# Optimization experiments

Measured on AMD Instinct MI355X. Metric: run time of the kernel, lower is better.

The kernel has to match this reference:

```python
import jax, jax.numpy as jnp
import numpy as np

B, S, D, H = 4, 2048, 1024, 16
HD = D // H


def setup_inputs() -> dict:
    key = jax.random.key(0)
    ks = jax.random.split(key, 6)
    scale = 1.0 / np.sqrt(D)
    return {
        'x': jax.random.normal(ks[0], (B, S, D), dtype=jnp.float32),
        'wq': jax.random.normal(ks[1], (D, D), dtype=jnp.float32) * scale,
        'wk': jax.random.normal(ks[2], (D, D), dtype=jnp.float32) * scale,
        'wv': jax.random.normal(ks[3], (D, D), dtype=jnp.float32) * scale,
        'wo': jax.random.normal(ks[4], (D, D), dtype=jnp.float32) * scale,
        'wo_b': jnp.zeros((D,), dtype=jnp.float32),
    }


def reference(x, wq, wk, wv, wo, wo_b):
    b, s, _ = x.shape
    # Linear projections (torch Linear: x @ W.T), reshape to [b, h, s, hd]
    def proj(w):
        return jnp.einsum('bsd,ed->bse', x, w).reshape(b, s, H, HD).transpose(0, 2, 1, 3)
    q, k, v = proj(wq), proj(wk), proj(wv)
    scores = jnp.einsum('bhqd,bhkd->bhqk', q, k)  # [b,h,s,s]
    causal = jnp.triu(jnp.ones((s, s), dtype=bool), k=1)
    scores = jnp.where(causal, -jnp.inf, scores)
    attn = jax.nn.softmax(scores / np.sqrt(HD), axis=-1)
    ctx = jnp.einsum('bhqk,bhkd->bhqd', attn, v)  # [b,h,s,hd]
    ctx = ctx.transpose(0, 2, 1, 3).reshape(b, s, D)
    return jnp.einsum('bsd,ed->bse', ctx, wo) + wo_b
```

## Files before the change

kernel.cpp:

```cpp
#include <hip/hip_runtime.h>

#define SB 4
#define SS 2048
#define SD 1024
#define SH 16
#define SHD 64
#define SM (SB * SS)

typedef __bf16 bf16x8 __attribute__((ext_vector_type(8)));
typedef float f32x4 __attribute__((ext_vector_type(4)));

static __device__ __forceinline__ unsigned short f2bf(float x) {
    unsigned int u = __builtin_bit_cast(unsigned int, x);
    u += 0x7fffu + ((u >> 16) & 1u);
    return (unsigned short)(u >> 16);
}

static __device__ __forceinline__ float fast_exp2(float x) {
#if __has_builtin(__builtin_amdgcn_exp2f)
    return __builtin_amdgcn_exp2f(x);
#else
    return exp2f(x);
#endif
}

static __device__ __forceinline__ unsigned int pkhi(float a, float b) {
    return __builtin_amdgcn_perm(__builtin_bit_cast(unsigned int, a),
                                 __builtin_bit_cast(unsigned int, b), 0x07060302u);
}

typedef __attribute__((address_space(1))) void GV;
typedef __attribute__((address_space(3))) void LV;

static __device__ __forceinline__ void async16(const void* g, void* l) {
    __builtin_amdgcn_global_load_lds((GV*)g, (LV*)l, 16, 0, 0);
}

#define QSCALE 0.18033688011112042f

__global__ __launch_bounds__(256) void cast_all(
    const float* __restrict__ x,  const float* __restrict__ wq,
    const float* __restrict__ wk, const float* __restrict__ wv,
    const float* __restrict__ wo,
    unsigned short* __restrict__ xb, unsigned short* __restrict__ wqkv,
    unsigned short* __restrict__ wo16) {
    int base = blockIdx.x * 512 + threadIdx.x;
#pragma unroll
    for (int it = 0; it < 2; ++it) {
        int i = base + it * 256;
        const float4* src;
        ushort4* dst;
        if (i < 2097152) {
            src = reinterpret_cast<const float4*>(x) + i;
            dst = reinterpret_cast<ushort4*>(xb) + i;
        } else {
            int j = i - 2097152;
            int which = j >> 18;
            int r = j & 262143;
            if (which == 0) {
                src = reinterpret_cast<const float4*>(wq) + r;
                dst = reinterpret_cast<ushort4*>(wqkv) + r;
            } else if (which == 1) {
                src = reinterpret_cast<const float4*>(wk) + r;
                dst = reinterpret_cast<ushort4*>(wqkv) + 262144 + r;
            } else if (which == 2) {
                src = reinterpret_cast<const float4*>(wv) + r;
                dst = reinterpret_cast<ushort4*>(wqkv) + 524288 + r;
            } else {
                src = reinterpret_cast<const float4*>(wo) + r;
                dst = reinterpret_cast<ushort4*>(wo16) + r;
            }
        }
        float4 v = *src;
        ushort4 o;
        o.x = f2bf(v.x); o.y = f2bf(v.y); o.z = f2bf(v.z); o.w = f2bf(v.w);
        *dst = o;
    }
}

#define NT16 (SD / 64)

__device__ __forceinline__ void gemm_mainloop(
    const unsigned short* __restrict__ A,
    const unsigned short* __restrict__ Bt,
    int tileM, int tileN, int tid,
    unsigned short* As0, unsigned short* As1, unsigned short* As2,
    unsigned short* Bs0, unsigned short* Bs1,
    f32x4 (&acc)[4][4]) {

    const int lane = tid & 63;
    const int quad = lane >> 4;
    const int col0 = lane & 15;
    const int w = tid >> 6;
    const int wm = w >> 1;
    const int wn = w & 1;

    const int r0 = tid >> 3;
    const int cc = ((tid & 7) ^ (r0 & 7)) * 8;

    const unsigned short* gA0 = A + (size_t)(tileM + r0) * SD + cc;
    const unsigned short* gA1 = gA0 + (size_t)64 * SD;
    const unsigned short* gA2 = gA0 + (size_t)128 * SD;
    const unsigned short* gA3 = gA0 + (size_t)192 * SD;
    const unsigned short* gB0 = Bt + (size_t)(tileN + r0) * SD + cc;
    const unsigned short* gB1 = gB0 + (size_t)64 * SD;

    unsigned short* const Asb[3] = {As0, As1, As2};
    unsigned short* const Bsb[2] = {Bs0, Bs1};
    const int t16 = tid * 16;

    const int cs0 = (quad ^ (col0 & 7)) * 16;
    const int cs1 = ((4 + quad) ^ (col0 & 7)) * 16;
    const int arow = (wm * 64 + col0) * 128;
    const int brow = (wn * 64 + col0) * 128;

#define STAGE_A(t, Asx) do {                                         \
        async16(gA0 + (t) * 64, (char*)(Asx) + t16);                 \
        async16(gA1 + (t) * 64, (char*)(Asx) + 8192 + t16);          \
        async16(gA2 + (t) * 64, (char*)(Asx) + 16384 + t16);         \
        async16(gA3 + (t) * 64, (char*)(Asx) + 24576 + t16);         \
    } while (0)
#define STAGE_B(t, Bsx) do {                                         \
        async16(gB0 + (t) * 64, (char*)(Bsx) + t16);                 \
        async16(gB1 + (t) * 64, (char*)(Bsx) + 8192 + t16);          \
    } while (0)

    STAGE_A(0, As0);
    STAGE_B(0, Bs0);
    STAGE_A(1, As1);

#pragma unroll
    for (int t = 0; t < NT16; ++t) {
        if (t + 1 < NT16)
            asm volatile("s_waitcnt vmcnt(4)" ::: "memory");
        else
            asm volatile("s_waitcnt vmcnt(0)" ::: "memory");
        __builtin_amdgcn_s_barrier();
        __builtin_amdgcn_sched_barrier(0);

        const unsigned short* As = Asb[t % 3];
        const unsigned short* Bs = Bsb[t & 1];

        bf16x8 af[4][2], bfr[4][2];
#pragma unroll
        for (int fr = 0; fr < 4; ++fr) {
            const char* rp = (const char*)As + arow + fr * 2048;
            af[fr][0] = *reinterpret_cast<const bf16x8*>(rp + cs0);
            af[fr][1] = *reinterpret_cast<const bf16x8*>(rp + cs1);
        }
#pragma unroll
        for (int fc = 0; fc < 4; ++fc) {
            const char* rp = (const char*)Bs + brow + fc * 2048;
            bfr[fc][0] = *reinterpret_cast<const bf16x8*>(rp + cs0);
            bfr[fc][1] = *reinterpret_cast<const bf16x8*>(rp + cs1);
        }

        if (t + 1 < NT16) STAGE_B(t + 1, Bsb[(t + 1) & 1]);
        if (t + 2 < NT16) STAGE_A(t + 2, Asb[(t + 2) % 3]);

        __builtin_amdgcn_s_setprio(1);
#pragma unroll
        for (int ks = 0; ks < 2; ++ks)
#pragma unroll
            for (int fr = 0; fr < 4; ++fr)
#pragma unroll
                for (int fc = 0; fc < 4; ++fc)
                    acc[fr][fc] = __builtin_amdgcn_mfma_f32_16x16x32_bf16(
                        af[fr][ks], bfr[fc][ks], acc[fr][fc], 0, 0, 0);
        __builtin_amdgcn_s_setprio(0);
    }
#undef STAGE_A
#undef STAGE_B
}

__global__ __launch_bounds__(512, 2) void gemm_qkv(
    const unsigned short* __restrict__ xb,
    const unsigned short* __restrict__ wqkv,
    unsigned short* __restrict__ Qd,
    unsigned short* __restrict__ Kd,
    unsigned short* __restrict__ Vtd) {

    __shared__ __align__(16) unsigned short As0[256 * 64];
    __shared__ __align__(16) unsigned short As1[256 * 64];
    __shared__ __align__(16) unsigned short As2[256 * 64];
    __shared__ __align__(16) unsigned short Bs0[128 * 64];
    __shared__ __align__(16) unsigned short Bs1[128 * 64];
    const int tid = threadIdx.x;
    const int tileN = blockIdx.x * 128;
    const int tileM = blockIdx.y * 256;

    f32x4 acc[4][4];
    const f32x4 z = {0.f, 0.f, 0.f, 0.f};
#pragma unroll
    for (int i = 0; i < 4; ++i)
#pragma unroll
        for (int j = 0; j < 4; ++j) acc[i][j] = z;

    gemm_mainloop(xb, wqkv, tileM, tileN, tid, As0, As1, As2, Bs0, Bs1, acc);

    const int lane = tid & 63, quad = lane >> 4, col0 = lane & 15;
    const int w = tid >> 6, wm = w >> 1, wn = w & 1;

#pragma unroll
    for (int ct = 0; ct < 4; ++ct) {
        int n0 = tileN + wn * 64 + ct * 16;
        int which = n0 >> 10;
        int e0 = n0 & 1023;
        int h = e0 >> 6;
        int hd = (e0 & 63) + col0;
#pragma unroll
        for (int rt = 0; rt < 4; ++rt) {
            int m0 = tileM + wm * 64 + rt * 16 + quad * 4;
            int bb = m0 >> 11;
            int s0 = m0 & 2047;
            int bh = bb * SH + h;
            if (which == 0) {
                int base = (bh * SS + s0) * SHD + hd;
#pragma unroll
                for (int r = 0; r < 4; ++r)
                    Qd[base + r * SHD] = f2bf(acc[rt][ct][r] * QSCALE);
            } else if (which == 1) {
                int base = (bh * SS + s0) * SHD + hd;
#pragma unroll
                for (int r = 0; r < 4; ++r)
                    Kd[base + r * SHD] = f2bf(acc[rt][ct][r]);
            } else {
                int base = (bh * SHD + hd) * SS + s0;
                ushort4 pk;
                pk.x = f2bf(acc[rt][ct][0]);
                pk.y = f2bf(acc[rt][ct][1]);
                pk.z = f2bf(acc[rt][ct][2]);
                pk.w = f2bf(acc[rt][ct][3]);
                *reinterpret_cast<ushort4*>(Vtd + base) = pk;
            }
        }
    }
}

__global__ __launch_bounds__(512, 2) void gemm_out(
    const unsigned short* __restrict__ ctx,
    const unsigned short* __restrict__ wo16,
    const float* __restrict__ wb,
    float* __restrict__ out) {

    __shared__ __align__(16) unsigned short As0[256 * 64];
    __shared__ __align__(16) unsigned short As1[256 * 64];
    __shared__ __align__(16) unsigned short As2[256 * 64];
    __shared__ __align__(16) unsigned short Bs0[128 * 64];
    __shared__ __align__(16) unsigned short Bs1[128 * 64];
    const int tid = threadIdx.x;
    const int tileN = blockIdx.x * 128;
    const int tileM = blockIdx.y * 256;

    f32x4 acc[4][4];
    const f32x4 z = {0.f, 0.f, 0.f, 0.f};
#pragma unroll
    for (int i = 0; i < 4; ++i)
#pragma unroll
        for (int j = 0; j < 4; ++j) acc[i][j] = z;

    gemm_mainloop(ctx, wo16, tileM, tileN, tid, As0, As1, As2, Bs0, Bs1, acc);

    const int lane = tid & 63, quad = lane >> 4, col0 = lane & 15;
    const int w = tid >> 6, wm = w >> 1, wn = w & 1;

#pragma unroll
    for (int ct = 0; ct < 4; ++ct) {
        int n = tileN + wn * 64 + ct * 16 + col0;
        float bias = wb[n];
#pragma unroll
        for (int rt = 0; rt < 4; ++rt) {
            int m0 = tileM + wm * 64 + rt * 16 + quad * 4;
#pragma unroll
            for (int r = 0; r < 4; ++r)
                out[(size_t)(m0 + r) * SD + n] = acc[rt][ct][r] + bias;
        }
    }
}

#define PSTR 72

__device__ __forceinline__ void stage_kv(
    const unsigned short* __restrict__ Kg,
    const unsigned short* __restrict__ Vtg,
    size_t base, int t, int srow0, int scs, int tid,
    unsigned short* Kb, unsigned short* Vb) {
#pragma unroll
    for (int j = 0; j < 2; ++j) {
        int row = j * 32 + srow0;
        int chunk = scs ^ (row & 7);
        int slot16 = (j * 256 + tid) * 16;
        async16(Kg + base + (size_t)(t * 64 + row) * SHD + chunk * 8,
                (char*)Kb + slot16);
        async16(Vtg + base + (size_t)row * SS + t * 64 + chunk * 8,
                (char*)Vb + slot16);
    }
}

__device__ __forceinline__ void attn_tile(
    const unsigned short* __restrict__ Kc,
    const unsigned short* __restrict__ Vc,
    int kb, int q0, int quad, int col0,
    const bf16x8 (&bq)[2][2], const bf16x8& ones,
    unsigned short* Psw, f32x4 (&ot)[2][4], f32x4 (&lacc)[2]) {

    const f32x4 z = {0.f, 0.f, 0.f, 0.f};

    bf16x8 ak[4][2];
#pragma unroll
    for (int rt = 0; rt < 4; ++rt)
#pragma unroll
        for (int ks = 0; ks < 2; ++ks)
            ak[rt][ks] = *reinterpret_cast<const bf16x8*>(
                &Kc[(rt * 16 + col0) * 64 + ((ks * 4 + quad) ^ (col0 & 7)) * 8]);

    f32x4 sc[2][4];
#pragma unroll
    for (int g = 0; g < 2; ++g)
#pragma unroll
        for (int rt = 0; rt < 4; ++rt) sc[g][rt] = z;
    __builtin_amdgcn_s_setprio(1);
#pragma unroll
    for (int rt = 0; rt < 4; ++rt)
#pragma unroll
        for (int g = 0; g < 2; ++g) {
            sc[g][rt] = __builtin_amdgcn_mfma_f32_16x16x32_bf16(
                ak[rt][0], bq[g][0], sc[g][rt], 0, 0, 0);
            sc[g][rt] = __builtin_amdgcn_mfma_f32_16x16x32_bf16(
                ak[rt][1], bq[g][1], sc[g][rt], 0, 0, 0);
        }
    __builtin_amdgcn_s_setprio(0);

    if (kb + 63 > q0) {
#pragma unroll
        for (int g = 0; g < 2; ++g) {
            int q = q0 + g * 16 + col0;
#pragma unroll
            for (int rt = 0; rt < 4; ++rt)
#pragma unroll
                for (int r = 0; r < 4; ++r) {
                    int key = kb + rt * 16 + quad * 4 + r;
                    if (key > q) sc[g][rt][r] = -3.0e38f;
                }
        }
    }

#pragma unroll
    for (int g = 0; g < 2; ++g)
#pragma unroll
        for (int rt = 0; rt < 4; ++rt)
#pragma unroll
            for (int r = 0; r < 4; ++r)
                sc[g][rt][r] = fast_exp2(sc[g][rt][r]);

    bf16x8 bp[2][2];
#pragma unroll
    for (int g = 0; g < 2; ++g) {
#pragma unroll
        for (int rt = 0; rt < 4; ++rt) {
            uint2 pk;
            pk.x = pkhi(sc[g][rt][1], sc[g][rt][0]);
            pk.y = pkhi(sc[g][rt][3], sc[g][rt][2]);
            *reinterpret_cast<uint2*>(&Psw[col0 * PSTR + rt * 16 + quad * 4]) = pk;
        }
#pragma unroll
        for (int ks = 0; ks < 2; ++ks)
            bp[g][ks] = *reinterpret_cast<const bf16x8*>(
                &Psw[col0 * PSTR + ks * 32 + quad * 8]);
    }

    __builtin_amdgcn_s_setprio(1);
#pragma unroll
    for (int ks = 0; ks < 2; ++ks) {
        lacc[0] = __builtin_amdgcn_mfma_f32_16x16x32_bf16(ones, bp[0][ks], lacc[0], 0, 0, 0);
        lacc[1] = __builtin_amdgcn_mfma_f32_16x16x32_bf16(ones, bp[1][ks], lacc[1], 0, 0, 0);
#pragma unroll
        for (int ct = 0; ct < 4; ++ct) {
            bf16x8 av = *reinterpret_cast<const bf16x8*>(
                &Vc[(ct * 16 + col0) * 64 + ((ks * 4 + quad) ^ (col0 & 7)) * 8]);
            ot[0][ct] = __builtin_amdgcn_mfma_f32_16x16x32_bf16(av, bp[0][ks], ot[0][ct], 0, 0, 0);
            ot[1][ct] = __builtin_amdgcn_mfma_f32_16x16x32_bf16(av, bp[1][ks], ot[1][ct], 0, 0, 0);
        }
    }
    __builtin_amdgcn_s_setprio(0);
}

__global__ __launch_bounds__(256) void attn_kernel(
    const unsigned short* __restrict__ Qg,
    const unsigned short* __restrict__ Kg,
    const unsigned short* __restrict__ Vtg,
    unsigned short* __restrict__ ctx) {

    __shared__ __align__(16) unsigned short K0[64 * 64];
    __shared__ __align__(16) unsigned short K1[64 * 64];
    __shared__ __align__(16) unsigned short V0[64 * 64];
    __shared__ __align__(16) unsigned short V1[64 * 64];
    __shared__ __align__(16) unsigned short Ps[4 * 16 * PSTR];

    const int tid = threadIdx.x;
    const int w = tid >> 6;
    const int lane = tid & 63;
    const int quad = lane >> 4;
    const int col0 = lane & 15;

    const int bh = (blockIdx.x << 3) | (blockIdx.y & 7);
    const int j2 = 15 - (blockIdx.y >> 3);

    const int b = bh >> 4;
    const int h = bh & 15;
    const size_t base = (size_t)bh * (SS * SHD);
    unsigned short* Psw = Ps + w * 16 * PSTR;

    bf16x8 ones;
#pragma unroll
    for (int i = 0; i < 8; ++i) ones[i] = (__bf16)1.0f;

    const int q0 = j2 * 128 + w * 32;
    const int qlim = q0 + 31;
    const int nkt = 2 * j2 + 2;

    bf16x8 bq[2][2];
#pragma unroll
    for (int g = 0; g < 2; ++g)
#pragma unroll
        for (int ks = 0; ks < 2; ++ks)
            bq[g][ks] = *reinterpret_cast<const bf16x8*>(
                Qg + base + (size_t)(q0 + g * 16 + col0) * SHD + ks * 32 + quad * 8);

    f32x4 ot[2][4], lacc[2];
    const f32x4 z = {0.f, 0.f, 0.f, 0.f};
#pragma unroll
    for (int g = 0; g < 2; ++g) {
        lacc[g] = z;
#pragma unroll
        for (int ct = 0; ct < 4; ++ct) ot[g][ct] = z;
    }

    const int srow0 = tid >> 3;
    const int scs = tid & 7;

    stage_kv(Kg, Vtg, base, 0, srow0, scs, tid, K0, V0);

#pragma unroll 1
    for (int kt = 0; kt < nkt; ++kt) {
        __syncthreads();
        if (kt + 1 < nkt) {
            if (kt & 1) stage_kv(Kg, Vtg, base, kt + 1, srow0, scs, tid, K0, V0);
            else        stage_kv(Kg, Vtg, base, kt + 1, srow0, scs, tid, K1, V1);
        }
        if (kt * 64 <= qlim) {
            const unsigned short* Kc = (kt & 1) ? K1 : K0;
            const unsigned short* Vc = (kt & 1) ? V1 : V0;
            attn_tile(Kc, Vc, kt * 64, q0, quad, col0, bq, ones, Psw, ot, lacc);
        }
    }

#pragma unroll
    for (int g = 0; g < 2; ++g) {
        float inv = 1.0f / lacc[g][0];
        int q = q0 + g * 16 + col0;
        size_t obase = ((size_t)b * SS + q) * SD + h * SHD;
#pragma unroll
        for (int ct = 0; ct < 4; ++ct) {
            uint2 pk;
            pk.x = pkhi(ot[g][ct][1] * inv, ot[g][ct][0] * inv);
            pk.y = pkhi(ot[g][ct][3] * inv, ot[g][ct][2] * inv);
            *reinterpret_cast<uint2*>(ctx + obase + ct * 16 + quad * 4) = pk;
        }
    }
}

extern "C" void kernel_launch(void* const* d_in, const int* in_sizes, int n_in,
                              void* d_out, int out_size, void* d_ws, size_t ws_size,
                              hipStream_t stream) {
    const float* x  = (const float*)d_in[0];
    const float* wq = (const float*)d_in[1];
    const float* wk = (const float*)d_in[2];
    const float* wv = (const float*)d_in[3];
    const float* wo = (const float*)d_in[4];
    const float* wb = (const float*)d_in[5];
    float* out = (float*)d_out;

    char* ws = (char*)d_ws;
    unsigned short* xb   = (unsigned short*)(ws + 0);
    unsigned short* wqkv = (unsigned short*)(ws + 16777216);
    unsigned short* q    = (unsigned short*)(ws + 23068672);
    unsigned short* k    = (unsigned short*)(ws + 39845888);
    unsigned short* vt   = (unsigned short*)(ws + 56623104);
    unsigned short* ctx  = (unsigned short*)(ws + 73400320);
    unsigned short* wo16 = (unsigned short*)(ws + 90177536);

    cast_all<<<6144, 256, 0, stream>>>(x, wq, wk, wv, wo, xb, wqkv, wo16);

    gemm_qkv<<<dim3(3 * SD / 128, SM / 256), 512, 0, stream>>>(xb, wqkv, q, k, vt);

    attn_kernel<<<dim3(8, 2 * SB * SH), 256, 0, stream>>>(q, k, vt, ctx);

    gemm_out<<<dim3(SD / 128, SM / 256), 512, 0, stream>>>(ctx, wo16, wb, out);
}
```

Before: 242.2 us.

## Pair light and heavy causal query blocks in one 512-thread attention workgroup

The attention kernel now launches 512-thread workgroups, half as many as before. Waves 0-3 handle query block jj and waves 4-7 handle the mirrored block 15-jj, so every workgroup does the same total causal work and shares one K/V staging stream. This balances load across workgroups and halves K/V global traffic and staging per pair. In exchange, the light half idles while the heavy half finishes its tiles, barriers now span 8 waves, and the launch-bounds hint may limit registers.

```diff
diff --git a/kernel.cpp b/kernel.cpp
--- a/kernel.cpp
+++ b/kernel.cpp
@@ -280,21 +280,18 @@
 
 #define PSTR 72
 
-__device__ __forceinline__ void stage_kv(
+__device__ __forceinline__ void stage_kv512(
     const unsigned short* __restrict__ Kg,
     const unsigned short* __restrict__ Vtg,
-    size_t base, int t, int srow0, int scs, int tid,
+    size_t base, int t, int tid,
     unsigned short* Kb, unsigned short* Vb) {
-#pragma unroll
-    for (int j = 0; j < 2; ++j) {
-        int row = j * 32 + srow0;
-        int chunk = scs ^ (row & 7);
-        int slot16 = (j * 256 + tid) * 16;
-        async16(Kg + base + (size_t)(t * 64 + row) * SHD + chunk * 8,
-                (char*)Kb + slot16);
-        async16(Vtg + base + (size_t)row * SS + t * 64 + chunk * 8,
-                (char*)Vb + slot16);
-    }
+    int row = tid >> 3;
+    int chunk = (tid & 7) ^ (row & 7);
+    int slot16 = tid * 16;
+    async16(Kg + base + (size_t)(t * 64 + row) * SHD + chunk * 8,
+            (char*)Kb + slot16);
+    async16(Vtg + base + (size_t)row * SS + t * 64 + chunk * 8,
+            (char*)Vb + slot16);
 }
 
 __device__ __forceinline__ void attn_tile(
@@ -385,7 +382,7 @@
     __builtin_amdgcn_s_setprio(0);
 }
 
-__global__ __launch_bounds__(256) void attn_kernel(
+__global__ __launch_bounds__(512, 6) void attn_kernel(
     const unsigned short* __restrict__ Qg,
     const unsigned short* __restrict__ Kg,
     const unsigned short* __restrict__ Vtg,
@@ -395,7 +392,7 @@
     __shared__ __align__(16) unsigned short K1[64 * 64];
     __shared__ __align__(16) unsigned short V0[64 * 64];
     __shared__ __align__(16) unsigned short V1[64 * 64];
-    __shared__ __align__(16) unsigned short Ps[4 * 16 * PSTR];
+    __shared__ __align__(16) unsigned short Ps[8 * 16 * PSTR];
 
     const int tid = threadIdx.x;
     const int w = tid >> 6;
@@ -404,7 +401,7 @@
     const int col0 = lane & 15;
 
     const int bh = (blockIdx.x << 3) | (blockIdx.y & 7);
-    const int j2 = 15 - (blockIdx.y >> 3);
+    const int jj = blockIdx.y >> 3;
 
     const int b = bh >> 4;
     const int h = bh & 15;
@@ -415,9 +412,10 @@
 #pragma unroll
     for (int i = 0; i < 8; ++i) ones[i] = (__bf16)1.0f;
 
-    const int q0 = j2 * 128 + w * 32;
+    const int q0 = (w < 4) ? (jj * 128 + w * 32)
+                           : ((15 - jj) * 128 + (w - 4) * 32);
     const int qlim = q0 + 31;
-    const int nkt = 2 * j2 + 2;
+    const int nkt = 32 - 2 * jj;
 
     bf16x8 bq[2][2];
 #pragma unroll
@@ -436,17 +434,14 @@
         for (int ct = 0; ct < 4; ++ct) ot[g][ct] = z;
     }
 
-    const int srow0 = tid >> 3;
-    const int scs = tid & 7;
-
-    stage_kv(Kg, Vtg, base, 0, srow0, scs, tid, K0, V0);
+    stage_kv512(Kg, Vtg, base, 0, tid, K0, V0);
 
 #pragma unroll 1
     for (int kt = 0; kt < nkt; ++kt) {
         __syncthreads();
         if (kt + 1 < nkt) {
-            if (kt & 1) stage_kv(Kg, Vtg, base, kt + 1, srow0, scs, tid, K0, V0);
-            else        stage_kv(Kg, Vtg, base, kt + 1, srow0, scs, tid, K1, V1);
+            if (kt & 1) stage_kv512(Kg, Vtg, base, kt + 1, tid, K0, V0);
+            else        stage_kv512(Kg, Vtg, base, kt + 1, tid, K1, V1);
         }
         if (kt * 64 <= qlim) {
             const unsigned short* Kc = (kt & 1) ? K1 : K0;
@@ -494,7 +489,7 @@
 
     gemm_qkv<<<dim3(3 * SD / 128, SM / 256), 512, 0, stream>>>(xb, wqkv, q, k, vt);
 
-    attn_kernel<<<dim3(8, 2 * SB * SH), 256, 0, stream>>>(q, k, vt, ctx);
+    attn_kernel<<<dim3(8, SB * SH), 512, 0, stream>>>(q, k, vt, ctx);
 
     gemm_out<<<dim3(SD / 128, SM / 256), 512, 0, stream>>>(ctx, wo16, wb, out);
 }
```

Measured after the change: 428.8 us. 1.77x slower.
